# Performance work log

Hardware: AMD Instinct MI355X
Metric: run time of the kernel (lower is better)

## Reference

```python
import jax, jax.numpy as jnp
import numpy as np

N = 100000   # num_nodes
E = 300000   # num directed edges (symmetrized to 2E inside forward)
D = 128      # input_dim
O = 128      # output_dim
R = 32       # num_relations
B = 8        # num_bases


def setup_inputs() -> dict:
    key = jax.random.key(0)
    ks = jax.random.split(key, 8)
    x = jax.random.normal(ks[0], (N, D), dtype=jnp.float32)
    node_keep_mask = jax.random.randint(ks[1], (N,), 0, 2) > 0
    source = jax.random.randint(ks[2], (E,), 0, N, dtype=jnp.int32)
    target = jax.random.randint(ks[3], (E,), 0, N, dtype=jnp.int32)
    edge_type = jax.random.randint(ks[4], (E,), 0, R, dtype=jnp.int32)
    edge_weights = jax.random.uniform(ks[5], (E,), dtype=jnp.float32)
    # xavier_normal for bases
    std = (2.0 / (D + O)) ** 0.5
    bases = jax.random.normal(ks[6], (B, D, O), dtype=jnp.float32) * std
    # uniform then L1-normalized rows, shape (R+1, B); row R is the self-loop
    rbw = jax.random.uniform(ks[7], (R + 1, B), dtype=jnp.float32)
    rbw = rbw / jnp.sum(rbw, axis=1, keepdims=True)
    return {
        "x": x,
        "node_keep_mask": node_keep_mask,
        "source": source,
        "target": target,
        "edge_type": edge_type,
        "edge_weights": edge_weights,
        "bases": bases,
        "relation_base_weights": rbw,
    }


def reference(x, node_keep_mask, source, target, edge_type, edge_weights,
              bases, relation_base_weights):
    # Self-loop: weight for relation id == num_relations (last row)
    w_self = jnp.einsum("bij,b->ij", bases, relation_base_weights[-1])
    out = jnp.where(node_keep_mask[:, None], x @ w_self, jnp.zeros((), x.dtype))

    # Symmetrize edges: messages flow in both directions (same relation/weight)
    src = jnp.concatenate([source, target])          # (2E,)
    tgt = jnp.concatenate([target, source])          # (2E,)
    etype = jnp.concatenate([edge_type, edge_type])  # (2E,)
    ew = jnp.concatenate([edge_weights, edge_weights])  # (2E,)

    # Project all nodes through every basis once: (N, B, O)
    proj = jnp.einsum("nd,bdo->nbo", x, bases)
    # Per-edge basis coefficients from the edge's relation: (2E, B)
    coeff = relation_base_weights[etype]
    # Message: x[src] @ (sum_b coeff_b * base_b) == sum_b coeff_b * proj[src, b]
    msg = jnp.einsum("eb,ebo->eo", coeff, proj[src])  # (2E, O)
    msg = msg * ew[:, None]

    # Scatter-add messages into target nodes
    out = out.at[tgt].add(msg)
    return out
```

## Files before the change

kernel.cpp:

```cpp
#include <hip/hip_runtime.h>

typedef __attribute__((ext_vector_type(8))) __bf16 bf16x8;
typedef __attribute__((ext_vector_type(4))) float f32x4;
typedef __attribute__((ext_vector_type(8))) unsigned short ushortx8;

__device__ inline unsigned short f2bf(float f) {
  unsigned int u = __float_as_uint(f);
  unsigned int r = (u + 0x7FFFu + ((u >> 16) & 1u)) >> 16;
  return (unsigned short)r;
}

__global__ __launch_bounds__(256) void prep_kernel(const float* __restrict__ x,
                                                   unsigned short* __restrict__ xb, int total8,
                                                   const float* __restrict__ bases,
                                                   unsigned short* __restrict__ bmt,
                                                   const unsigned char* __restrict__ mask,
                                                   int mbytes, int* __restrict__ flag_out,
                                                   int CB, int TB) {
  int bid = blockIdx.x;
  if (bid < CB) {
    int id = bid * 256 + threadIdx.x;
    if (id >= total8) return;
    f32x4 f0 = ((const f32x4*)x)[2 * id];
    f32x4 f1 = ((const f32x4*)x)[2 * id + 1];
    ushortx8 r;
    r[0] = f2bf(f0[0]); r[1] = f2bf(f0[1]); r[2] = f2bf(f0[2]); r[3] = f2bf(f0[3]);
    r[4] = f2bf(f1[0]); r[5] = f2bf(f1[1]); r[6] = f2bf(f1[2]); r[7] = f2bf(f1[3]);
    ((ushortx8*)xb)[id] = r;
  } else if (bid < CB + TB) {
    int id = (bid - CB) * 256 + threadIdx.x;
    if (id >= 128 * 1024) return;
    int o = id >> 10, k = id & 1023, b = k >> 7, d = k & 127;
    bmt[id] = f2bf(bases[b * 16384 + d * 128 + o]);
  } else {
    __shared__ int nz_off, big;
    if (threadIdx.x == 0) { nz_off = 0; big = 0; }
    __syncthreads();
    int lnz = 0, lbig = 0;
    for (int i = threadIdx.x; i < mbytes; i += 256) {
      unsigned char v = mask[i];
      if ((i & 3) && v) lnz++;
      if (v > 1) lbig++;
    }
    if (lnz) atomicAdd(&nz_off, lnz);
    if (lbig) atomicAdd(&big, lbig);
    __syncthreads();
    if (threadIdx.x == 0) *flag_out = (nz_off == 0) ? 0 : ((big == 0) ? 1 : 2);
  }
}

__global__ __launch_bounds__(256) void hist_kernel(const int* __restrict__ src,
                                                   const int* __restrict__ tgt, int E,
                                                   int* __restrict__ cnt) {
  int i = blockIdx.x * 256 + threadIdx.x;
  if (i >= E) return;
  atomicAdd(&cnt[tgt[i]], 1);
  atomicAdd(&cnt[src[i]], 1);
}

__global__ __launch_bounds__(256) void scan1_kernel(const int* __restrict__ cnt, int N,
                                                    int* __restrict__ bsum) {
  __shared__ int s[256];
  int t = threadIdx.x, i = blockIdx.x * 256 + t;
  s[t] = (i < N) ? cnt[i] : 0;
  __syncthreads();
#pragma unroll
  for (int off = 128; off > 0; off >>= 1) {
    if (t < off) s[t] += s[t + off];
    __syncthreads();
  }
  if (t == 0) bsum[blockIdx.x] = s[0];
}

__global__ void scan2_kernel(const int* __restrict__ bsum, int nb,
                             int* __restrict__ bexcl, int* __restrict__ base, int N) {
  __shared__ int s[512];
  int t = threadIdx.x;
  int v = (t < nb) ? bsum[t] : 0;
  s[t] = v;
  __syncthreads();
  for (int off = 1; off < 512; off <<= 1) {
    int x = (t >= off) ? s[t - off] : 0;
    __syncthreads();
    s[t] += x;
    __syncthreads();
  }
  if (t < nb) bexcl[t] = s[t] - v;
  if (t == nb - 1) base[N] = s[t];
}

__global__ __launch_bounds__(256) void scan3_kernel(const int* __restrict__ cnt, int N,
                                                    const int* __restrict__ bexcl,
                                                    int* __restrict__ base,
                                                    int* __restrict__ cursor) {
  __shared__ int s[256];
  int t = threadIdx.x, i = blockIdx.x * 256 + t;
  int c = (i < N) ? cnt[i] : 0;
  s[t] = c;
  __syncthreads();
  for (int off = 1; off < 256; off <<= 1) {
    int x = (t >= off) ? s[t - off] : 0;
    __syncthreads();
    s[t] += x;
    __syncthreads();
  }
  if (i < N) {
    int v = bexcl[blockIdx.x] + s[t] - c;
    base[i] = v;
    cursor[i] = v;
  }
}

__global__ __launch_bounds__(256) void scatter_kernel(const int* __restrict__ src,
                                                      const int* __restrict__ tgt,
                                                      const int* __restrict__ et,
                                                      const float* __restrict__ ew, int E,
                                                      int* __restrict__ cursor,
                                                      uint2* __restrict__ msrw) {
  int i = blockIdx.x * 256 + threadIdx.x;
  if (i >= E) return;
  int s = src[i], g = tgt[i], r = et[i];
  unsigned wbits = __float_as_uint(ew[i]);
  int s1 = atomicAdd(&cursor[g], 1);
  msrw[s1] = make_uint2((unsigned)s | ((unsigned)r << 24), wbits);
  int s2 = atomicAdd(&cursor[s], 1);
  msrw[s2] = make_uint2((unsigned)g | ((unsigned)r << 24), wbits);
}

__global__ __launch_bounds__(512, 4) void gather_kernel(
    const unsigned* __restrict__ xb32, const unsigned short* __restrict__ bmt,
    const int* __restrict__ base, const uint2* __restrict__ msrw,
    const float* __restrict__ rbw, const void* __restrict__ maskp,
    const int* __restrict__ flag_p, float* __restrict__ out, int N) {
  extern __shared__ char smem[];
  float* ctab = (float*)(smem + 65536);
  int t = threadIdx.x;
  for (int i = t; i < 264; i += 512) ctab[i] = rbw[i];
  int wid = t >> 6, l = t & 63;
  int t0 = blockIdx.x * 32;
  int flag = *flag_p;
  __syncthreads();

  int tgbase = t0 + wid * 4;
  int bv = 0;
  if (l < 5) bv = base[min(tgbase + (int)l, N)];
  int baseArr[5];
#pragma unroll
  for (int j = 0; j < 5; ++j) baseArr[j] = __shfl(bv, j);

  unsigned xself[4];
  float msk[4];
#pragma unroll
  for (int j = 0; j < 4; ++j) {
    int tg = tgbase + j;
    int tgc = min(tg, N - 1);
    xself[j] = xb32[(size_t)tgc * 64 + l];
    bool keep;
    if (flag == 0)      keep = ((const int*)maskp)[tgc] != 0;
    else if (flag == 1) keep = ((const unsigned char*)maskp)[tgc] != 0;
    else                keep = ((const float*)maskp)[tgc] != 0.f;
    msk[j] = (keep && tg < N) ? 1.f : 0.f;
  }

  uint2 srwl = make_uint2(0u, 0u);
  {
    int c = (tgbase < N) ? (baseArr[1] - baseArr[0]) : 0;
    if (c > 0) srwl = msrw[baseArr[0] + min((int)l, c - 1)];
  }

  for (int j = 0; j < 4; ++j) {
    int tg = tgbase + j;
    int beg = baseArr[j];
    int cnt = (tg < N) ? (baseArr[j + 1] - beg) : 0;
    float zlo[8], zhi[8];
    {
      float slo = __uint_as_float(xself[j] << 16);
      float shi = __uint_as_float(xself[j] & 0xFFFF0000u);
#pragma unroll
      for (int b = 0; b < 8; ++b) {
        float a = msk[j] * ctab[256 + b];
        zlo[b] = a * slo;
        zhi[b] = a * shi;
      }
    }
    uint2 cur = srwl;
    if (j < 3) {
      int cn = (tg + 1 < N) ? (baseArr[j + 2] - baseArr[j + 1]) : 0;
      srwl = make_uint2(0u, 0u);
      if (cn > 0) srwl = msrw[baseArr[j + 1] + min((int)l, cn - 1)];
    }
    for (int mb = 0; mb < cnt; mb += 64) {
      if (mb > 0) cur = msrw[beg + mb + min((int)l, cnt - mb - 1)];
      int blk = min(cnt - mb, 64);
      for (int c0 = 0; c0 < blk; c0 += 8) {
        unsigned sx[8], xr[8];
        float wv[8];
#pragma unroll
        for (int s = 0; s < 8; ++s) {
          int m = c0 + s;
          int msel = (m < blk) ? m : 0;
          unsigned a = __shfl(cur.x, msel);
          unsigned wb = __shfl(cur.y, msel);
          sx[s] = a;
          wv[s] = (m < blk) ? __uint_as_float(wb) : 0.f;
          unsigned row = (m < blk) ? (a & 0xFFFFFFu) : 0u;
          xr[s] = xb32[(size_t)row * 64 + l];
        }
#pragma unroll
        for (int s = 0; s < 8; ++s) {
          int rel = (int)(sx[s] >> 24);
          f32x4 cA = *(const f32x4*)&ctab[rel * 8];
          f32x4 cB = *(const f32x4*)&ctab[rel * 8 + 4];
          float cc[8] = {cA[0], cA[1], cA[2], cA[3], cB[0], cB[1], cB[2], cB[3]};
          float lo = __uint_as_float(xr[s] << 16);
          float hi = __uint_as_float(xr[s] & 0xFFFF0000u);
          float w = wv[s];
#pragma unroll
          for (int b = 0; b < 8; ++b) {
            float a = w * cc[b];
            zlo[b] = fmaf(a, lo, zlo[b]);
            zhi[b] = fmaf(a, hi, zhi[b]);
          }
        }
      }
    }
    int row = wid * 4 + j;
#pragma unroll
    for (int b = 0; b < 8; ++b) {
      unsigned pk = (unsigned)f2bf(zlo[b]) | ((unsigned)f2bf(zhi[b]) << 16);
      int byte = row * 2048 + ((b * 256 + l * 4) ^ ((row & 7) << 4));
      *(unsigned*)(smem + byte) = pk;
    }
  }
  __syncthreads();

  int l15 = l & 15, lk8 = (l >> 4) * 8;
  f32x4 acc[2] = {};
  for (int ks = 0; ks < 32; ++ks) {
    int k0 = ks * 32 + lk8;
    bf16x8 a[2], bb;
#pragma unroll
    for (int rt = 0; rt < 2; ++rt) {
      int tr = rt * 16 + l15;
      int byte = tr * 2048 + ((k0 * 2) ^ ((tr & 7) << 4));
      a[rt] = *(const bf16x8*)(smem + byte);
    }
    int col = wid * 16 + l15;
    bb = *(const bf16x8*)(bmt + (size_t)col * 1024 + k0);
#pragma unroll
    for (int rt = 0; rt < 2; ++rt)
      acc[rt] = __builtin_amdgcn_mfma_f32_16x16x32_bf16(a[rt], bb, acc[rt], 0, 0, 0);
  }
#pragma unroll
  for (int rt = 0; rt < 2; ++rt) {
    int rowb = t0 + rt * 16 + (l >> 4) * 4;
    int col = wid * 16 + l15;
#pragma unroll
    for (int i = 0; i < 4; ++i) {
      int row = rowb + i;
      if (row < N) out[(size_t)row * 128 + col] = acc[rt][i];
    }
  }
}

extern "C" void kernel_launch(void* const* d_in, const int* in_sizes, int n_in,
                              void* d_out, int out_size, void* d_ws, size_t ws_size,
                              hipStream_t stream) {
  const float* x = (const float*)d_in[0];
  const void* mask = d_in[1];
  const int* source = (const int*)d_in[2];
  const int* target = (const int*)d_in[3];
  const int* etype = (const int*)d_in[4];
  const float* eweight = (const float*)d_in[5];
  const float* bases = (const float*)d_in[6];
  const float* rbw = (const float*)d_in[7];
  float* out = (float*)d_out;

  const int N = in_sizes[1];
  const int E = in_sizes[2];
  const int M = 2 * E;
  const int NB = (N + 255) / 256;

  char* ws = (char*)d_ws;
  size_t off = 0;
  unsigned short* xb = (unsigned short*)(ws + off); off += (size_t)N * 256;
  unsigned short* bmt = (unsigned short*)(ws + off); off += 128 * 1024 * 2;
  uint2* msrw = (uint2*)(ws + off); off += (size_t)(M + 4) * 8;
  int* base = (int*)(ws + off); off += ((size_t)N + 64) * 4;
  int* cursor = (int*)(ws + off); off += ((size_t)N + 64) * 4;
  int* cnt = (int*)(ws + off); off += ((size_t)N + 64) * 4;
  int* bsum = (int*)(ws + off); off += 2048;
  int* bexcl = (int*)(ws + off); off += 2048;
  int* flag = (int*)(ws + off); off += 256;

  hipMemsetAsync(cnt, 0, (size_t)N * 4, stream);
  int total8 = (N * 128) / 8;
  int CB = (total8 + 255) / 256;
  int TB = (128 * 1024 + 255) / 256;
  prep_kernel<<<CB + TB + 1, 256, 0, stream>>>(x, xb, total8, bases, bmt,
                                               (const unsigned char*)mask,
                                               N < 8192 ? N : 8192, flag, CB, TB);
  hist_kernel<<<(E + 255) / 256, 256, 0, stream>>>(source, target, E, cnt);
  scan1_kernel<<<NB, 256, 0, stream>>>(cnt, N, bsum);
  scan2_kernel<<<1, 512, 0, stream>>>(bsum, NB, bexcl, base, N);
  scan3_kernel<<<NB, 256, 0, stream>>>(cnt, N, bexcl, base, cursor);
  scatter_kernel<<<(E + 255) / 256, 256, 0, stream>>>(source, target, etype, eweight, E,
                                                      cursor, msrw);
  int gblk = (N + 31) / 32;
  size_t shmem = 65536 + 264 * sizeof(float) + 16;
  gather_kernel<<<gblk, 512, shmem, stream>>>((const unsigned*)xb, bmt, base, msrw,
                                              rbw, mask, flag, out, N);
}
```

Measured before the change: 279.9 us.

## Use 1024-thread gather blocks with scalar edge loads and global coefficient reads

Doubles the gather block to 1024 threads so each wave aggregates two target nodes instead of four. Edge records are read with wave-uniform loads rather than lane-distributed loads plus shuffles. The relation coefficient table is read directly from global memory instead of being staged in LDS. The MFMA epilogue gives each wave one 16x16 tile. The aim is more parallelism and less shuffle overhead, at the risk of register pressure from the aggressive launch bounds and less latency hiding per wave.

```diff
diff --git a/kernel.cpp b/kernel.cpp
--- a/kernel.cpp
+++ b/kernel.cpp
@@ -127,104 +127,70 @@
   msrw[s2] = make_uint2((unsigned)g | ((unsigned)r << 24), wbits);
 }
 
-__global__ __launch_bounds__(512, 4) void gather_kernel(
+__global__ __launch_bounds__(1024, 8) void gather_kernel(
     const unsigned* __restrict__ xb32, const unsigned short* __restrict__ bmt,
     const int* __restrict__ base, const uint2* __restrict__ msrw,
     const float* __restrict__ rbw, const void* __restrict__ maskp,
     const int* __restrict__ flag_p, float* __restrict__ out, int N) {
   extern __shared__ char smem[];
-  float* ctab = (float*)(smem + 65536);
   int t = threadIdx.x;
-  for (int i = t; i < 264; i += 512) ctab[i] = rbw[i];
   int wid = t >> 6, l = t & 63;
   int t0 = blockIdx.x * 32;
   int flag = *flag_p;
-  __syncthreads();
-
-  int tgbase = t0 + wid * 4;
-  int bv = 0;
-  if (l < 5) bv = base[min(tgbase + (int)l, N)];
-  int baseArr[5];
-#pragma unroll
-  for (int j = 0; j < 5; ++j) baseArr[j] = __shfl(bv, j);
-
-  unsigned xself[4];
-  float msk[4];
-#pragma unroll
-  for (int j = 0; j < 4; ++j) {
-    int tg = tgbase + j;
+
+  for (int j = 0; j < 2; ++j) {
+    int tg = __builtin_amdgcn_readfirstlane(t0 + wid * 2 + j);
     int tgc = min(tg, N - 1);
-    xself[j] = xb32[(size_t)tgc * 64 + l];
-    bool keep;
+    int beg = __builtin_amdgcn_readfirstlane(base[tgc]);
+    int cnt = __builtin_amdgcn_readfirstlane(base[tgc + 1]) - beg;
+    if (tg >= N) cnt = 0;
+    unsigned xs = xb32[(size_t)tgc * 64 + l];
+    int keep;
     if (flag == 0)      keep = ((const int*)maskp)[tgc] != 0;
     else if (flag == 1) keep = ((const unsigned char*)maskp)[tgc] != 0;
     else                keep = ((const float*)maskp)[tgc] != 0.f;
-    msk[j] = (keep && tg < N) ? 1.f : 0.f;
-  }
-
-  uint2 srwl = make_uint2(0u, 0u);
-  {
-    int c = (tgbase < N) ? (baseArr[1] - baseArr[0]) : 0;
-    if (c > 0) srwl = msrw[baseArr[0] + min((int)l, c - 1)];
-  }
-
-  for (int j = 0; j < 4; ++j) {
-    int tg = tgbase + j;
-    int beg = baseArr[j];
-    int cnt = (tg < N) ? (baseArr[j + 1] - beg) : 0;
+    float ms = (keep && tg < N) ? 1.f : 0.f;
+    float slo = __uint_as_float(xs << 16);
+    float shi = __uint_as_float(xs & 0xFFFF0000u);
     float zlo[8], zhi[8];
-    {
-      float slo = __uint_as_float(xself[j] << 16);
-      float shi = __uint_as_float(xself[j] & 0xFFFF0000u);
-#pragma unroll
-      for (int b = 0; b < 8; ++b) {
-        float a = msk[j] * ctab[256 + b];
-        zlo[b] = a * slo;
-        zhi[b] = a * shi;
+#pragma unroll
+    for (int b = 0; b < 8; ++b) {
+      float a = ms * rbw[256 + b];
+      zlo[b] = a * slo;
+      zhi[b] = a * shi;
+    }
+    for (int mb = 0; mb < cnt; mb += 8) {
+      unsigned rowv[8];
+      float wv[8];
+      int relv[8];
+#pragma unroll
+      for (int s = 0; s < 8; ++s) {
+        int m = mb + s;
+        uint2 mm = msrw[beg + m];
+        int valid = m < cnt;
+        unsigned mx = valid ? mm.x : 0u;
+        rowv[s] = mx & 0xFFFFFFu;
+        relv[s] = (int)(mx >> 24);
+        wv[s] = valid ? __uint_as_float(mm.y) : 0.f;
       }
-    }
-    uint2 cur = srwl;
-    if (j < 3) {
-      int cn = (tg + 1 < N) ? (baseArr[j + 2] - baseArr[j + 1]) : 0;
-      srwl = make_uint2(0u, 0u);
-      if (cn > 0) srwl = msrw[baseArr[j + 1] + min((int)l, cn - 1)];
-    }
-    for (int mb = 0; mb < cnt; mb += 64) {
-      if (mb > 0) cur = msrw[beg + mb + min((int)l, cnt - mb - 1)];
-      int blk = min(cnt - mb, 64);
-      for (int c0 = 0; c0 < blk; c0 += 8) {
-        unsigned sx[8], xr[8];
-        float wv[8];
-#pragma unroll
-        for (int s = 0; s < 8; ++s) {
-          int m = c0 + s;
-          int msel = (m < blk) ? m : 0;
-          unsigned a = __shfl(cur.x, msel);
-          unsigned wb = __shfl(cur.y, msel);
-          sx[s] = a;
-          wv[s] = (m < blk) ? __uint_as_float(wb) : 0.f;
-          unsigned row = (m < blk) ? (a & 0xFFFFFFu) : 0u;
-          xr[s] = xb32[(size_t)row * 64 + l];
-        }
-#pragma unroll
-        for (int s = 0; s < 8; ++s) {
-          int rel = (int)(sx[s] >> 24);
-          f32x4 cA = *(const f32x4*)&ctab[rel * 8];
-          f32x4 cB = *(const f32x4*)&ctab[rel * 8 + 4];
-          float cc[8] = {cA[0], cA[1], cA[2], cA[3], cB[0], cB[1], cB[2], cB[3]};
-          float lo = __uint_as_float(xr[s] << 16);
-          float hi = __uint_as_float(xr[s] & 0xFFFF0000u);
-          float w = wv[s];
-#pragma unroll
-          for (int b = 0; b < 8; ++b) {
-            float a = w * cc[b];
-            zlo[b] = fmaf(a, lo, zlo[b]);
-            zhi[b] = fmaf(a, hi, zhi[b]);
-          }
+      unsigned xr[8];
+#pragma unroll
+      for (int s = 0; s < 8; ++s) xr[s] = xb32[(size_t)rowv[s] * 64 + l];
+#pragma unroll
+      for (int s = 0; s < 8; ++s) {
+        const float* cc = rbw + relv[s] * 8;
+        float lo = __uint_as_float(xr[s] << 16);
+        float hi = __uint_as_float(xr[s] & 0xFFFF0000u);
+        float w = wv[s];
+#pragma unroll
+        for (int b = 0; b < 8; ++b) {
+          float a = w * cc[b];
+          zlo[b] = fmaf(a, lo, zlo[b]);
+          zhi[b] = fmaf(a, hi, zhi[b]);
         }
       }
     }
-    int row = wid * 4 + j;
+    int row = wid * 2 + j;
 #pragma unroll
     for (int b = 0; b < 8; ++b) {
       unsigned pk = (unsigned)f2bf(zlo[b]) | ((unsigned)f2bf(zhi[b]) << 16);
@@ -235,31 +201,21 @@
   __syncthreads();
 
   int l15 = l & 15, lk8 = (l >> 4) * 8;
-  f32x4 acc[2] = {};
+  int rt = wid >> 3, c8 = wid & 7;
+  f32x4 acc = {};
   for (int ks = 0; ks < 32; ++ks) {
     int k0 = ks * 32 + lk8;
-    bf16x8 a[2], bb;
-#pragma unroll
-    for (int rt = 0; rt < 2; ++rt) {
-      int tr = rt * 16 + l15;
-      int byte = tr * 2048 + ((k0 * 2) ^ ((tr & 7) << 4));
-      a[rt] = *(const bf16x8*)(smem + byte);
-    }
-    int col = wid * 16 + l15;
-    bb = *(const bf16x8*)(bmt + (size_t)col * 1024 + k0);
-#pragma unroll
-    for (int rt = 0; rt < 2; ++rt)
-      acc[rt] = __builtin_amdgcn_mfma_f32_16x16x32_bf16(a[rt], bb, acc[rt], 0, 0, 0);
-  }
-#pragma unroll
-  for (int rt = 0; rt < 2; ++rt) {
-    int rowb = t0 + rt * 16 + (l >> 4) * 4;
-    int col = wid * 16 + l15;
-#pragma unroll
-    for (int i = 0; i < 4; ++i) {
-      int row = rowb + i;
-      if (row < N) out[(size_t)row * 128 + col] = acc[rt][i];
-    }
+    int tr = rt * 16 + l15;
+    bf16x8 a = *(const bf16x8*)(smem + tr * 2048 + ((k0 * 2) ^ ((tr & 7) << 4)));
+    bf16x8 bb = *(const bf16x8*)(bmt + (size_t)(c8 * 16 + l15) * 1024 + k0);
+    acc = __builtin_amdgcn_mfma_f32_16x16x32_bf16(a, bb, acc, 0, 0, 0);
+  }
+  int rowb = t0 + rt * 16 + (l >> 4) * 4;
+  int col = c8 * 16 + l15;
+#pragma unroll
+  for (int i = 0; i < 4; ++i) {
+    int row = rowb + i;
+    if (row < N) out[(size_t)row * 128 + col] = acc[i];
   }
 }
 
@@ -285,7 +241,7 @@
   size_t off = 0;
   unsigned short* xb = (unsigned short*)(ws + off); off += (size_t)N * 256;
   unsigned short* bmt = (unsigned short*)(ws + off); off += 128 * 1024 * 2;
-  uint2* msrw = (uint2*)(ws + off); off += (size_t)(M + 4) * 8;
+  uint2* msrw = (uint2*)(ws + off); off += (size_t)(M + 16) * 8;
   int* base = (int*)(ws + off); off += ((size_t)N + 64) * 4;
   int* cursor = (int*)(ws + off); off += ((size_t)N + 64) * 4;
   int* cnt = (int*)(ws + off); off += ((size_t)N + 64) * 4;
@@ -307,7 +263,7 @@
   scatter_kernel<<<(E + 255) / 256, 256, 0, stream>>>(source, target, etype, eweight, E,
                                                       cursor, msrw);
   int gblk = (N + 31) / 32;
-  size_t shmem = 65536 + 264 * sizeof(float) + 16;
-  gather_kernel<<<gblk, 512, shmem, stream>>>((const unsigned*)xb, bmt, base, msrw,
-                                              rbw, mask, flag, out, N);
-}
+  size_t shmem = 65536;
+  gather_kernel<<<gblk, 1024, shmem, stream>>>((const unsigned*)xb, bmt, base, msrw,
+                                               rbw, mask, flag, out, N);
+}
```

Result: slower. 327.3 us (+16.9%).
